# Optimization experiments

Hardware: AMD Instinct MI355X
Metric: run time of the kernel (lower is better)

## Reference

```python
import jax, jax.numpy as jnp
import numpy as np

INPUT_SIZE = 64
HIDDEN_SIZE = 128
OUTPUT_SIZE = 64


def setup_inputs() -> dict:
    key = jax.random.key(0)
    ks = jax.random.split(key, 7)
    B, T = 256, 2048
    x = jax.random.normal(ks[0], (B, T, INPUT_SIZE), dtype=jnp.float32)
    s_in = 1.0 / np.sqrt(INPUT_SIZE)
    s_h = 1.0 / np.sqrt(HIDDEN_SIZE)
    Wx_w = jax.random.uniform(ks[1], (HIDDEN_SIZE, INPUT_SIZE), minval=-s_in, maxval=s_in, dtype=jnp.float32)
    Wx_b = jax.random.uniform(ks[2], (HIDDEN_SIZE,), minval=-s_in, maxval=s_in, dtype=jnp.float32)
    Wh_w = jax.random.uniform(ks[3], (HIDDEN_SIZE, HIDDEN_SIZE), minval=-s_h, maxval=s_h, dtype=jnp.float32)
    Wh_b = jax.random.uniform(ks[4], (HIDDEN_SIZE,), minval=-s_h, maxval=s_h, dtype=jnp.float32)
    fc_w = jax.random.uniform(ks[5], (OUTPUT_SIZE, HIDDEN_SIZE), minval=-s_h, maxval=s_h, dtype=jnp.float32)
    fc_b = jax.random.uniform(ks[6], (OUTPUT_SIZE,), minval=-s_h, maxval=s_h, dtype=jnp.float32)
    return {"x": x, "Wx_w": Wx_w, "Wx_b": Wx_b, "Wh_w": Wh_w, "Wh_b": Wh_b, "fc_w": fc_w, "fc_b": fc_b}


def reference(x, Wx_w, Wx_b, Wh_w, Wh_b, fc_w, fc_b):
    B = x.shape[0]
    # Precompute the input projection for all timesteps in one big GEMM;
    # the recurrence itself is a scan over time (sequential dependency).
    xt_proj = jnp.einsum('bti,hi->bth', x, Wx_w) + Wx_b  # [B, T, H]

    def step(h, xp):
        h = jnp.tanh(xp + h @ Wh_w.T + Wh_b)
        return h, None

    h0 = jnp.zeros((B, HIDDEN_SIZE), dtype=x.dtype)
    h_final, _ = jax.lax.scan(step, h0, jnp.swapaxes(xt_proj, 0, 1))  # scan over T
    out = h_final @ fc_w.T + fc_b  # [B, O]
    return jax.nn.softmax(out, axis=1)
```

## Files before the change

### kernel.cpp

```cpp
#include <hip/hip_runtime.h>

#define BATCH 256
#define TSTEPS 2048
#define INSZ 64
#define HID 128
#define OUTSZ 64
#define CHUNK 16
#define NCHUNK (TSTEPS / CHUNK)

typedef float v2f __attribute__((ext_vector_type(2)));
typedef float v4f __attribute__((ext_vector_type(4)));

#define AS1 __attribute__((address_space(1)))
#define AS3 __attribute__((address_space(3)))

template <int CTRL>
__device__ __forceinline__ float dppf(float v) {
  return __int_as_float(__builtin_amdgcn_update_dpp(
      0, __float_as_int(v), CTRL, 0xF, 0xF, true));
}
#define DPP_XOR1 0xB1
#define DPP_XOR2 0x4E
#define DPP_XOR15 0x140
#define DPP_XOR8 0x128

__launch_bounds__(256, 1)
__global__ void rnn_dpp_kernel(const float* __restrict__ x,
                               const float* __restrict__ Wx_w,
                               const float* __restrict__ Wx_b,
                               const float* __restrict__ Wh_w,
                               const float* __restrict__ Wh_b,
                               const float* __restrict__ fc_w,
                               const float* __restrict__ fc_b,
                               float* __restrict__ out) {
  const int b = blockIdx.x;
  const int tid = threadIdx.x;
  const int l = tid & 63;
  const int s = tid & 15;
  const int g = tid >> 4;
  const int l0 = l & 1, l1 = (l >> 1) & 1, l2 = (l >> 2) & 1;
  const int ii = (l0 ^ l2) | ((l1 ^ l2) << 1) | (l2 << 2);
  const int jf = 8 * g + ii;

  __shared__ __align__(16) float hA[192], hB[192];
  __shared__ __align__(16) float xsm[2][CHUNK * INSZ];

  v2f wh2[8][4], wx2[8][2];
#pragma unroll
  for (int m = 0; m < 8; ++m) {
    const int row = 8 * g + (m ^ ii);
    const float* p = Wh_w + row * HID + 8 * s;
    v4f t0 = *(const v4f*)p;
    v4f t1 = *(const v4f*)(p + 4);
    wh2[m][0] = (v2f){t0.x, t0.y};
    wh2[m][1] = (v2f){t0.z, t0.w};
    wh2[m][2] = (v2f){t1.x, t1.y};
    wh2[m][3] = (v2f){t1.z, t1.w};
    const float* q = Wx_w + row * INSZ + 4 * s;
    v4f t2 = *(const v4f*)q;
    wx2[m][0] = (v2f){t2.x, t2.y};
    wx2[m][1] = (v2f){t2.z, t2.w};
  }
#pragma unroll
  for (int m = 0; m < 8; ++m) {
#pragma unroll
    for (int kk = 0; kk < 4; ++kk) asm volatile("" : "+v"(wh2[m][kk]));
#pragma unroll
    for (int kk = 0; kk < 2; ++kk) asm volatile("" : "+v"(wx2[m][kk]));
  }
  const float bc = Wx_b[jf] + Wh_b[jf];

  const float* xg = x + (size_t)b * TSTEPS * INSZ;

  if (tid < 192) hA[tid] = 0.f;

  {
    const AS1 float* gp = (const AS1 float*)(xg + tid * 4);
    AS3 float* d = (AS3 float*)(&xsm[0][(tid >> 6) * 256]);
    __builtin_amdgcn_global_load_lds(gp, d, 16, 0, 0);
  }
  asm volatile("s_waitcnt vmcnt(0) lgkmcnt(0)\ns_barrier" ::: "memory");

  for (int tc = 0; tc < NCHUNK; ++tc) {
    if (tc + 1 < NCHUNK) {
      const AS1 float* gp =
          (const AS1 float*)(xg + (size_t)(tc + 1) * CHUNK * INSZ + tid * 4);
      AS3 float* d = (AS3 float*)(&xsm[(tc + 1) & 1][(tid >> 6) * 256]);
      __builtin_amdgcn_global_load_lds(gp, d, 16, 0, 0);
    }
    const float* xc = xsm[tc & 1];

#pragma unroll
    for (int ts = 0; ts < CHUNK; ++ts) {
      const float* hin = (ts & 1) ? hB : hA;
      float* hout = (ts & 1) ? hA : hB;

      v4f xv = *(const v4f*)&xc[ts * INSZ + 4 * s];
      const float* hp = hin + 12 * s;
      v4f h0 = *(const v4f*)hp;
      v4f h1 = *(const v4f*)(hp + 4);

      v2f hx0 = (v2f){h0.x, h0.y}, hx1 = (v2f){h0.z, h0.w};
      v2f hx2 = (v2f){h1.x, h1.y}, hx3 = (v2f){h1.z, h1.w};
      v2f xx0 = (v2f){xv.x, xv.y}, xx1 = (v2f){xv.z, xv.w};

      float a0, a1, a2, a3, a4, a5, a6, a7;
      float* aptr[8] = {&a0, &a1, &a2, &a3, &a4, &a5, &a6, &a7};
#pragma unroll
      for (int m = 0; m < 8; ++m) {
        v2f acc = wh2[m][0] * hx0;
        acc = __builtin_elementwise_fma(wh2[m][1], hx1, acc);
        acc = __builtin_elementwise_fma(wh2[m][2], hx2, acc);
        acc = __builtin_elementwise_fma(wh2[m][3], hx3, acc);
        acc = __builtin_elementwise_fma(wx2[m][0], xx0, acc);
        acc = __builtin_elementwise_fma(wx2[m][1], xx1, acc);
        *aptr[m] = acc.x + acc.y;
      }

      float b0 = a0 + dppf<DPP_XOR1>(a1);
      float b1 = a2 + dppf<DPP_XOR1>(a3);
      float b2 = a4 + dppf<DPP_XOR1>(a5);
      float b3 = a6 + dppf<DPP_XOR1>(a7);
      float c0 = b0 + dppf<DPP_XOR2>(b1);
      float c1 = b2 + dppf<DPP_XOR2>(b3);
      float dd = c0 + dppf<DPP_XOR15>(c1);
      float z  = dd + dppf<DPP_XOR8>(dd);

      z += bc;
      float e = __builtin_amdgcn_exp2f(z * 2.8853900817779268f);
      float hn = 1.f - 2.f * __builtin_amdgcn_rcpf(e + 1.f);

      if ((l & 8) == 0) hout[12 * g + ii] = hn;

      if (ts == CHUNK - 1) {
        asm volatile("s_waitcnt vmcnt(0) lgkmcnt(0)\ns_barrier" ::: "memory");
      } else {
        asm volatile("s_waitcnt lgkmcnt(0)\ns_barrier" ::: "memory");
      }
    }
  }

  if (tid < 64) {
    float acc = fc_b[tid];
    const float* fr = fc_w + tid * HID;
#pragma unroll
    for (int k8 = 0; k8 < 16; ++k8) {
      v4f w0 = *(const v4f*)(fr + 8 * k8);
      v4f w1 = *(const v4f*)(fr + 8 * k8 + 4);
      const float* hh = &hA[12 * k8];
      v4f p0 = *(const v4f*)hh;
      v4f p1 = *(const v4f*)(hh + 4);
      acc = fmaf(w0.x, p0.x, acc);
      acc = fmaf(w0.y, p0.y, acc);
      acc = fmaf(w0.z, p0.z, acc);
      acc = fmaf(w0.w, p0.w, acc);
      acc = fmaf(w1.x, p1.x, acc);
      acc = fmaf(w1.y, p1.y, acc);
      acc = fmaf(w1.z, p1.z, acc);
      acc = fmaf(w1.w, p1.w, acc);
    }
    float m = acc;
#pragma unroll
    for (int off = 32; off >= 1; off >>= 1) m = fmaxf(m, __shfl_xor(m, off, 64));
    float e = __builtin_amdgcn_exp2f((acc - m) * 1.4426950408889634f);
    float ssum = e;
#pragma unroll
    for (int off = 32; off >= 1; off >>= 1) ssum += __shfl_xor(ssum, off, 64);
    out[b * OUTSZ + tid] = e / ssum;
  }
}

extern "C" void kernel_launch(void* const* d_in, const int* in_sizes, int n_in,
                              void* d_out, int out_size, void* d_ws, size_t ws_size,
                              hipStream_t stream) {
  const float* x    = (const float*)d_in[0];
  const float* Wx_w = (const float*)d_in[1];
  const float* Wx_b = (const float*)d_in[2];
  const float* Wh_w = (const float*)d_in[3];
  const float* Wh_b = (const float*)d_in[4];
  const float* fc_w = (const float*)d_in[5];
  const float* fc_b = (const float*)d_in[6];
  float* out = (float*)d_out;

  rnn_dpp_kernel<<<BATCH, 256, 0, stream>>>(x, Wx_w, Wx_b, Wh_w, Wh_b, fc_w, fc_b, out);
}
```

Before: 551.5 us.

## Split recurrence across 512 threads with 4 outputs per thread group

Doubles the block to 512 threads so each 16-lane group computes 4 hidden units instead of 8. This halves the per-step FMA chain and shortens the DPP reduction tree on the serial critical path. It also doubles the x chunk size to 32, prefetches the next x vector from LDS one step ahead, and forces packed FMA via inline asm. The cost is a barrier across 8 waves instead of 4 each step, plus more LDS writers and a larger shared x buffer.

```diff
diff --git a/kernel.cpp b/kernel.cpp
--- a/kernel.cpp
+++ b/kernel.cpp
@@ -5,7 +5,8 @@
 #define INSZ 64
 #define HID 128
 #define OUTSZ 64
-#define CHUNK 16
+#define NTHR 512
+#define CHUNK 32
 #define NCHUNK (TSTEPS / CHUNK)
 
 typedef float v2f __attribute__((ext_vector_type(2)));
@@ -24,31 +25,38 @@
 #define DPP_XOR15 0x140
 #define DPP_XOR8 0x128
 
-__launch_bounds__(256, 1)
-__global__ void rnn_dpp_kernel(const float* __restrict__ x,
-                               const float* __restrict__ Wx_w,
-                               const float* __restrict__ Wx_b,
-                               const float* __restrict__ Wh_w,
-                               const float* __restrict__ Wh_b,
-                               const float* __restrict__ fc_w,
-                               const float* __restrict__ fc_b,
-                               float* __restrict__ out) {
+__device__ __forceinline__ v2f pk_mul(v2f a, v2f b) {
+  v2f d; asm("v_pk_mul_f32 %0, %1, %2" : "=v"(d) : "v"(a), "v"(b)); return d;
+}
+__device__ __forceinline__ v2f pk_fma(v2f a, v2f b, v2f c) {
+  v2f d; asm("v_pk_fma_f32 %0, %1, %2, %3" : "=v"(d) : "v"(a), "v"(b), "v"(c)); return d;
+}
+
+__launch_bounds__(NTHR, 1)
+__global__ void rnn_dpp512_kernel(const float* __restrict__ x,
+                                  const float* __restrict__ Wx_w,
+                                  const float* __restrict__ Wx_b,
+                                  const float* __restrict__ Wh_w,
+                                  const float* __restrict__ Wh_b,
+                                  const float* __restrict__ fc_w,
+                                  const float* __restrict__ fc_b,
+                                  float* __restrict__ out) {
   const int b = blockIdx.x;
   const int tid = threadIdx.x;
-  const int l = tid & 63;
   const int s = tid & 15;
   const int g = tid >> 4;
-  const int l0 = l & 1, l1 = (l >> 1) & 1, l2 = (l >> 2) & 1;
-  const int ii = (l0 ^ l2) | ((l1 ^ l2) << 1) | (l2 << 2);
-  const int jf = 8 * g + ii;
+  const int s0 = s & 1, s1 = (s >> 1) & 1, s2 = (s >> 2) & 1;
+  const int c = (s0 ^ s2) | ((s1 ^ s2) << 1);
+  const int jf = 4 * g + c;
+  const int jp = jf + ((jf >> 3) << 2);
 
   __shared__ __align__(16) float hA[192], hB[192];
   __shared__ __align__(16) float xsm[2][CHUNK * INSZ];
 
-  v2f wh2[8][4], wx2[8][2];
+  v2f wh2[4][4], wx2[4][2];
 #pragma unroll
-  for (int m = 0; m < 8; ++m) {
-    const int row = 8 * g + (m ^ ii);
+  for (int m = 0; m < 4; ++m) {
+    const int row = 4 * g + (m ^ c);
     const float* p = Wh_w + row * HID + 8 * s;
     v4f t0 = *(const v4f*)p;
     v4f t1 = *(const v4f*)(p + 4);
@@ -60,13 +68,6 @@
     v4f t2 = *(const v4f*)q;
     wx2[m][0] = (v2f){t2.x, t2.y};
     wx2[m][1] = (v2f){t2.z, t2.w};
-  }
-#pragma unroll
-  for (int m = 0; m < 8; ++m) {
-#pragma unroll
-    for (int kk = 0; kk < 4; ++kk) asm volatile("" : "+v"(wh2[m][kk]));
-#pragma unroll
-    for (int kk = 0; kk < 2; ++kk) asm volatile("" : "+v"(wx2[m][kk]));
   }
   const float bc = Wx_b[jf] + Wh_b[jf];
 
@@ -82,6 +83,13 @@
   asm volatile("s_waitcnt vmcnt(0) lgkmcnt(0)\ns_barrier" ::: "memory");
 
   for (int tc = 0; tc < NCHUNK; ++tc) {
+#pragma unroll
+    for (int m = 0; m < 4; ++m) {
+#pragma unroll
+      for (int kk = 0; kk < 4; ++kk) asm("" : "+v"(wh2[m][kk]));
+#pragma unroll
+      for (int kk = 0; kk < 2; ++kk) asm("" : "+v"(wx2[m][kk]));
+    }
     if (tc + 1 < NCHUNK) {
       const AS1 float* gp =
           (const AS1 float*)(xg + (size_t)(tc + 1) * CHUNK * INSZ + tid * 4);
@@ -89,48 +97,50 @@
       __builtin_amdgcn_global_load_lds(gp, d, 16, 0, 0);
     }
     const float* xc = xsm[tc & 1];
+    v4f xcur = *(const v4f*)&xc[4 * s];
 
 #pragma unroll
     for (int ts = 0; ts < CHUNK; ++ts) {
       const float* hin = (ts & 1) ? hB : hA;
       float* hout = (ts & 1) ? hA : hB;
 
-      v4f xv = *(const v4f*)&xc[ts * INSZ + 4 * s];
       const float* hp = hin + 12 * s;
       v4f h0 = *(const v4f*)hp;
       v4f h1 = *(const v4f*)(hp + 4);
 
+      v4f xnext;
+      if (ts + 1 < CHUNK) xnext = *(const v4f*)&xc[(ts + 1) * INSZ + 4 * s];
+
+      v2f xx0 = (v2f){xcur.x, xcur.y}, xx1 = (v2f){xcur.z, xcur.w};
       v2f hx0 = (v2f){h0.x, h0.y}, hx1 = (v2f){h0.z, h0.w};
       v2f hx2 = (v2f){h1.x, h1.y}, hx3 = (v2f){h1.z, h1.w};
-      v2f xx0 = (v2f){xv.x, xv.y}, xx1 = (v2f){xv.z, xv.w};
 
-      float a0, a1, a2, a3, a4, a5, a6, a7;
-      float* aptr[8] = {&a0, &a1, &a2, &a3, &a4, &a5, &a6, &a7};
+      float a0, a1, a2, a3;
+      float* aptr[4] = {&a0, &a1, &a2, &a3};
 #pragma unroll
-      for (int m = 0; m < 8; ++m) {
-        v2f acc = wh2[m][0] * hx0;
-        acc = __builtin_elementwise_fma(wh2[m][1], hx1, acc);
-        acc = __builtin_elementwise_fma(wh2[m][2], hx2, acc);
-        acc = __builtin_elementwise_fma(wh2[m][3], hx3, acc);
-        acc = __builtin_elementwise_fma(wx2[m][0], xx0, acc);
-        acc = __builtin_elementwise_fma(wx2[m][1], xx1, acc);
+      for (int m = 0; m < 4; ++m) {
+        v2f acc = pk_mul(wx2[m][0], xx0);
+        acc = pk_fma(wx2[m][1], xx1, acc);
+        acc = pk_fma(wh2[m][0], hx0, acc);
+        acc = pk_fma(wh2[m][1], hx1, acc);
+        acc = pk_fma(wh2[m][2], hx2, acc);
+        acc = pk_fma(wh2[m][3], hx3, acc);
         *aptr[m] = acc.x + acc.y;
       }
 
       float b0 = a0 + dppf<DPP_XOR1>(a1);
       float b1 = a2 + dppf<DPP_XOR1>(a3);
-      float b2 = a4 + dppf<DPP_XOR1>(a5);
-      float b3 = a6 + dppf<DPP_XOR1>(a7);
-      float c0 = b0 + dppf<DPP_XOR2>(b1);
-      float c1 = b2 + dppf<DPP_XOR2>(b3);
-      float dd = c0 + dppf<DPP_XOR15>(c1);
-      float z  = dd + dppf<DPP_XOR8>(dd);
+      float w  = b0 + dppf<DPP_XOR2>(b1);
+      float u  = w + dppf<DPP_XOR15>(w);
+      float z  = u + dppf<DPP_XOR8>(u);
 
       z += bc;
       float e = __builtin_amdgcn_exp2f(z * 2.8853900817779268f);
-      float hn = 1.f - 2.f * __builtin_amdgcn_rcpf(e + 1.f);
+      float hn = fmaf(-2.f, __builtin_amdgcn_rcpf(e + 1.f), 1.f);
 
-      if ((l & 8) == 0) hout[12 * g + ii] = hn;
+      if (s < 4) hout[jp] = hn;
+
+      if (ts + 1 < CHUNK) xcur = xnext;
 
       if (ts == CHUNK - 1) {
         asm volatile("s_waitcnt vmcnt(0) lgkmcnt(0)\ns_barrier" ::: "memory");
@@ -182,5 +192,5 @@
   const float* fc_b = (const float*)d_in[6];
   float* out = (float*)d_out;
 
-  rnn_dpp_kernel<<<BATCH, 256, 0, stream>>>(x, Wx_w, Wx_b, Wh_w, Wh_b, fc_w, fc_b, out);
+  rnn_dpp512_kernel<<<BATCH, NTHR, 0, stream>>>(x, Wx_w, Wx_b, Wh_w, Wh_b, fc_w, fc_b, out);
 }
```

Measured after the change: 538.8 us (median of 2 runs). 1.02x faster.
